# Kernel tuning notes

Measured on AMD Instinct MI355X. Metric: run time of the kernel, lower is better.

## Reference

```python
import jax, jax.numpy as jnp
import numpy as np

N = 50000
E = 800000
D = 16            # input_dim == hidden_dim == output_dim (required for consistency)
D2 = D * D
HEADS = 4
NEG_SLOPE = 0.2


def _gat_conv(x, src, dst, W, att_src, att_dst, bias):
    """PyG GATConv with concat=False (mean over heads), add_self_loops already applied.
    x: [N, Cin], W: [Cin, H*C], att_*: [H, C], bias: [C]."""
    H, C = att_src.shape
    xh = (x @ W).reshape(N, H, C)                     # [N, H, C]
    a_src = jnp.einsum('nhc,hc->nh', xh, att_src)      # [N, H]
    a_dst = jnp.einsum('nhc,hc->nh', xh, att_dst)
    alpha = jax.nn.leaky_relu(a_src[src] + a_dst[dst], NEG_SLOPE)   # [E, H]
    amax = jax.ops.segment_max(alpha, dst, num_segments=N)
    amax = jnp.where(jnp.isfinite(amax), amax, 0.0)
    ex = jnp.exp(alpha - jax.lax.stop_gradient(amax)[dst])
    denom = jax.ops.segment_sum(ex, dst, num_segments=N)
    coef = ex / (denom[dst] + 1e-16)                  # per-dst softmax over incoming edges
    acc = jnp.zeros((N, C), x.dtype)
    for h in range(H):  # loop over heads to avoid [E, H, C] intermediate
        acc = acc + jax.ops.segment_sum(coef[:, h:h + 1] * xh[src, h], dst, num_segments=N)
    return acc / H + bias


def setup_inputs() -> dict:
    key = jax.random.key(0)
    ks = jax.random.split(key, 20)
    s = lambda k, shape, fan: jax.random.normal(k, shape, jnp.float32) * (1.0 / np.sqrt(fan))
    inp = {
        'mean': jax.random.normal(ks[0], (N, D), jnp.float32),
        'cov': jax.random.normal(ks[1], (N, D, D), jnp.float32),
        'edge_index': jax.random.randint(ks[2], (2, E), 0, N, jnp.int32),
        # gat_mean params
        'W_mean': s(ks[3], (D, HEADS * D), D),
        'att_src_mean': s(ks[4], (HEADS, D), D),
        'att_dst_mean': s(ks[5], (HEADS, D), D),
        'bias_mean': jnp.zeros((D,), jnp.float32),
        # gat_cov params
        'W_cov': s(ks[6], (D2, HEADS * D2), D2),
        'att_src_cov': s(ks[7], (HEADS, D2), D2),
        'att_dst_cov': s(ks[8], (HEADS, D2), D2),
        'bias_cov': jnp.zeros((D2,), jnp.float32),
        # fc_mean: Linear(D,D) -> Linear(D,D)
        'fm_W1': s(ks[9], (D, D), D), 'fm_b1': jnp.zeros((D,), jnp.float32),
        'fm_W2': s(ks[10], (D, D), D), 'fm_b2': jnp.zeros((D,), jnp.float32),
        # fc_cov: Linear(D2,D2) -> Linear(D2,D2)
        'fcv_W1': s(ks[11], (D2, D2), D2), 'fcv_b1': jnp.zeros((D2,), jnp.float32),
        'fcv_W2': s(ks[12], (D2, D2), D2), 'fcv_b2': jnp.zeros((D2,), jnp.float32),
    }
    return inp


def reference(mean, cov, edge_index, W_mean, att_src_mean, att_dst_mean, bias_mean,
              W_cov, att_src_cov, att_dst_cov, bias_cov,
              fm_W1, fm_b1, fm_W2, fm_b2, fcv_W1, fcv_b1, fcv_W2, fcv_b2):
    loops = jnp.arange(N, dtype=edge_index.dtype)
    src = jnp.concatenate([edge_index[0], loops])
    dst = jnp.concatenate([edge_index[1], loops])

    cov_flat = cov.reshape(N, D2)
    mean_agg = _gat_conv(mean, src, dst, W_mean, att_src_mean, att_dst_mean, bias_mean)
    cov_agg = _gat_conv(cov_flat, src, dst, W_cov, att_src_cov, att_dst_cov, bias_cov)

    mean_out = (mean_agg @ fm_W1 + fm_b1) @ fm_W2 + fm_b2
    cov_out = (cov_agg @ fcv_W1 + fcv_b1) @ fcv_W2 + fcv_b2
    return mean_out, cov_out.reshape(N, D, D)
```

## Files before the change

### kernel.cpp

```cpp
#include <hip/hip_runtime.h>

#define NN 50000
#define EE 800000
#define DD 16
#define DD2 256
#define ETOT (EE + NN)
#define NB 196

typedef __bf16 bf16x8 __attribute__((ext_vector_type(8)));
typedef float f32x4 __attribute__((ext_vector_type(4)));
typedef float f32x2 __attribute__((ext_vector_type(2)));

__device__ inline unsigned short f2bf(float f) {
    unsigned int u = __float_as_uint(f);
    return (unsigned short)((u + 0x7FFFu + ((u >> 16) & 1u)) >> 16);
}

__device__ inline void gl2lds16(const void* g, void* l) {
    __builtin_amdgcn_global_load_lds((const __attribute__((address_space(1))) unsigned int*)g,
                                     (__attribute__((address_space(3))) unsigned int*)l, 16, 0, 0);
}

__global__ void k_count(const int* ei, int* counts) {
    int e = blockIdx.x * 256 + threadIdx.x;
    if (e < EE) atomicAdd(&counts[ei[EE + e]], 1);
}

__global__ void k_scan1(const int* counts, int* partial, int* bsum) {
    __shared__ int sh[256];
    int t = threadIdx.x;
    int n = blockIdx.x * 256 + t;
    int v = (n < NN) ? counts[n] + 1 : 0;
    sh[t] = v;
    __syncthreads();
    for (int d = 1; d < 256; d <<= 1) {
        int x = (t >= d) ? sh[t - d] : 0;
        __syncthreads();
        sh[t] += x;
        __syncthreads();
    }
    if (n < NN) partial[n] = sh[t];
    if (t == 255) bsum[blockIdx.x] = sh[255];
}

__global__ void k_scan3(const int* counts, const int* partial, const int* bsum,
                        int* row_start, int* cursor) {
    __shared__ int sh[256];
    int t = threadIdx.x;
    int v = (t < NB) ? bsum[t] : 0;
    sh[t] = v;
    __syncthreads();
    for (int d = 1; d < 256; d <<= 1) {
        int x = (t >= d) ? sh[t - d] : 0;
        __syncthreads();
        sh[t] += x;
        __syncthreads();
    }
    int boff = (blockIdx.x == 0) ? 0 : sh[blockIdx.x - 1];
    int n = blockIdx.x * 256 + t;
    if (n < NN) {
        int rs = partial[n] - (counts[n] + 1) + boff;
        row_start[n] = rs;
        cursor[n] = rs;
        if (n == NN - 1) row_start[NN] = partial[n] + boff;
    }
}

__global__ void k_scatter(const int* ei, int* cursor, int* srt) {
    int i = blockIdx.x * 256 + threadIdx.x;
    if (i >= ETOT) return;
    int s, d;
    if (i < EE) { s = ei[i]; d = ei[EE + i]; }
    else { s = d = i - EE; }
    int pos = atomicAdd(&cursor[d], 1);
    srt[pos] = s;
}

__global__ void k_pre(const float* fcv_W1, const float* fcv_W2, const float* fcv_b1, const float* fcv_b2,
                      const float* fm_W1, const float* fm_W2, const float* fm_b1, const float* fm_b2,
                      const float* W_cov, const float* as_cov, const float* ad_cov,
                      const float* W_mean, const float* as_mean, const float* ad_mean,
                      const float* bias_cov, const float* bias_mean,
                      unsigned short* WpT, float* bpc, float* vcov, float* vmean,
                      float* Wpm, float* bpm) {
    __shared__ float sh[256];
    int b = blockIdx.x, t = threadIdx.x;
    if (b < 1024) {
        int q = b >> 8, i = b & 255;
        const float* wrow = W_cov + (size_t)i * 1024 + q * 256;
        float t1 = 0.f;
        for (int j = 0; j < 256; ++j) t1 += wrow[j] * fcv_W1[j * 256 + t];
        sh[t] = t1;
        __syncthreads();
        float s = 0.f;
        for (int k = 0; k < 256; ++k) s += sh[k] * fcv_W2[k * 256 + t];
        int C = q * 32 + (i >> 3);
        int cs = C ^ (t & 7);
        WpT[(size_t)t * 1024 + cs * 8 + (i & 7)] = f2bf(0.25f * s);
    } else if (b == 1024) {
        float t1 = fcv_b1[t];
        for (int j = 0; j < 256; ++j) t1 += bias_cov[j] * fcv_W1[j * 256 + t];
        sh[t] = t1;
        __syncthreads();
        float s = fcv_b2[t];
        for (int k = 0; k < 256; ++k) s += sh[k] * fcv_W2[k * 256 + t];
        bpc[t] = s;
    } else if (b < 1033) {
        int ch = b - 1025, h = ch & 3;
        const float* att = (ch < 4) ? as_cov : ad_cov;
        int jl = t & 31, i8 = t >> 5;
        float av[8];
#pragma unroll
        for (int jj = 0; jj < 8; ++jj) av[jj] = att[h * 256 + jj * 32 + jl];
        for (int ii = 0; ii < 32; ++ii) {
            int i = ii * 8 + i8;
            const float* wr = W_cov + (size_t)i * 1024 + h * 256;
            float p = 0.f;
#pragma unroll
            for (int jj = 0; jj < 8; ++jj) p += wr[jj * 32 + jl] * av[jj];
#pragma unroll
            for (int off = 16; off; off >>= 1) p += __shfl_xor(p, off);
            if (jl == 0) vcov[ch * 256 + i] = p;
        }
    } else {
        {
            int j = t >> 4, c = t & 15;
            float s = 0.f;
            for (int k = 0; k < 16; ++k) s += fm_W1[j * 16 + k] * fm_W2[k * 16 + c];
            sh[j * 16 + c] = s;
        }
        if (t < 128) {
            int ch = t >> 4, i = t & 15, h = ch & 3;
            const float* att = (ch < 4) ? as_mean : ad_mean;
            float s = 0.f;
            for (int j = 0; j < 16; ++j) s += W_mean[i * 64 + h * 16 + j] * att[h * 16 + j];
            vmean[ch * 16 + i] = s;
        }
        __syncthreads();
#pragma unroll
        for (int r = 0; r < 4; ++r) {
            int idx = r * 256 + t;
            int k = idx >> 4, c = idx & 15, h = k >> 4, i = k & 15;
            float s = 0.f;
            for (int j = 0; j < 16; ++j) s += W_mean[i * 64 + h * 16 + j] * sh[j * 16 + c];
            Wpm[k * 16 + c] = 0.25f * s;
        }
        if (t < 16) {
            float b2 = fm_b2[t];
            for (int k = 0; k < 16; ++k) b2 += fm_b1[k] * fm_W2[k * 16 + t];
            float s = b2;
            for (int j = 0; j < 16; ++j) s += bias_mean[j] * sh[j * 16 + t];
            bpm[t] = s;
        }
    }
}

__global__ void __launch_bounds__(256) k_dots(const float* cov, const float* mean,
                                              const float* vcov, const float* vmean,
                                              float* asrc, float* adst, unsigned short* covb) {
    __shared__ float vc[8 * 256];
    __shared__ float vm[8 * 16];
    int t = threadIdx.x;
    for (int i = t; i < 2048; i += 256) vc[i] = vcov[i];
    if (t < 128) vm[t] = vmean[t];
    __syncthreads();
    int w = t >> 6, lane = t & 63;
    int n = blockIdx.x * 4 + w;
    float4 x = *(const float4*)(cov + (size_t)n * 256 + lane * 4);
    unsigned int u0 = (unsigned int)f2bf(x.x) | ((unsigned int)f2bf(x.y) << 16);
    unsigned int u1 = (unsigned int)f2bf(x.z) | ((unsigned int)f2bf(x.w) << 16);
    *(uint2*)((char*)covb + (size_t)n * 512 + lane * 8) = make_uint2(u0, u1);
    float p[8];
#pragma unroll
    for (int c = 0; c < 8; ++c) {
        float4 v = *(const float4*)&vc[c * 256 + lane * 4];
        p[c] = x.x * v.x + x.y * v.y + x.z * v.z + x.w * v.w;
    }
#pragma unroll
    for (int c = 0; c < 8; ++c)
        for (int off = 32; off; off >>= 1) p[c] += __shfl_xor(p[c], off);
    float xm = (lane < 16) ? mean[(size_t)n * 16 + lane] : 0.f;
    float q[8];
#pragma unroll
    for (int c = 0; c < 8; ++c) {
        q[c] = (lane < 16) ? xm * vm[c * 16 + lane] : 0.f;
        for (int off = 8; off; off >>= 1) q[c] += __shfl_xor(q[c], off);
    }
    if (lane == 0) {
        float4* ps = (float4*)(asrc + (size_t)n * 8);
        ps[0] = make_float4(p[0], p[1], p[2], p[3]);
        ps[1] = make_float4(q[0], q[1], q[2], q[3]);
        float4* pd = (float4*)(adst + (size_t)n * 8);
        pd[0] = make_float4(p[4], p[5], p[6], p[7]);
        pd[1] = make_float4(q[4], q[5], q[6], q[7]);
    }
}

__global__ void __launch_bounds__(256, 8) k_agg(const int* __restrict__ row_start, const int* __restrict__ srt,
                                                const float* __restrict__ asrc, const float* __restrict__ adst,
                                                const unsigned short* __restrict__ covb, const float* __restrict__ mean,
                                                unsigned short* __restrict__ Ycat, float* __restrict__ Ym) {
    __shared__ float exbuf[4][64][8];
    __shared__ float mrow[4][64][16];
    int t = threadIdx.x;
    int w = t >> 6, lane = t & 63;
    int ml = lane & 15;
    int hl4 = lane >> 4;
    const char* covbc = (const char*)covb;
    const char* meanc = (const char*)mean;
    const char* asrcc = (const char*)asrc;
    unsigned lodc = (unsigned)lane << 3;
    float* exw = &exbuf[w][0][0];
    float* mrw = &mrow[w][0][0];

    for (int n0 = blockIdx.x * 4; n0 < NN; n0 += gridDim.x * 4) {
        int nu = __builtin_amdgcn_readfirstlane(n0 + w);
        int beg = row_start[nu], deg = row_start[nu + 1] - beg;

        f32x2 acc[8];
#pragma unroll
        for (int k = 0; k < 8; ++k) acc[k] = (f32x2){0.f, 0.f};
        float accm = 0.f;
        float dsc[4] = {0, 0, 0, 0};
        float dsm = 0.f;

        auto loadg = [&](int jp, int s0v, uint2* cd) {
#pragma unroll
            for (int k2 = 0; k2 < 4; ++k2) {
                int se = __shfl(s0v, jp + k2);
                cd[k2] = *(const uint2*)(covbc + (((unsigned)se << 9) + lodc));
            }
        };
        auto compute4 = [&](int jp, const uint2* cd) {
#pragma unroll
            for (int k2 = 0; k2 < 4; ++k2) {
                int e = jp + k2;
                float4 e0 = *(const float4*)(exw + e * 8);
                float em = exw[e * 8 + 4 + hl4];
                float mv = mrw[e * 16 + (ml ^ ((e & 7) << 1))];
                f32x2 x0 = (f32x2){__uint_as_float(cd[k2].x << 16), __uint_as_float(cd[k2].x & 0xffff0000u)};
                f32x2 x1 = (f32x2){__uint_as_float(cd[k2].y << 16), __uint_as_float(cd[k2].y & 0xffff0000u)};
                float ev[4] = {e0.x, e0.y, e0.z, e0.w};
#pragma unroll
                for (int h = 0; h < 4; ++h) {
                    f32x2 e2 = (f32x2){ev[h], ev[h]};
                    acc[h * 2 + 0] = __builtin_elementwise_fma(e2, x0, acc[h * 2 + 0]);
                    acc[h * 2 + 1] = __builtin_elementwise_fma(e2, x1, acc[h * 2 + 1]);
                }
                dsc[0] += e0.x; dsc[1] += e0.y; dsc[2] += e0.z; dsc[3] += e0.w;
                accm += em * mv;
                dsm += em;
            }
        };

        for (int base = 0; base < deg; base += 64) {
            int i = base + lane;
            bool valid = i < deg;
            int s0 = srt[beg + (valid ? i : (deg - 1))];
            int cnt8 = (min(64, deg - base) + 7) & ~7;

            uint2 cdA[4], cdB[4];
            loadg(0, s0, cdA);
            loadg(4, s0, cdB);

            {
                const float4* pm = (const float4*)(meanc + ((size_t)((unsigned)s0 << 6)));
                bool oddE = lane & 1;
                int g0 = (lane >> 1) & 3;
                float* mb = mrw + lane * 16;
                float4 F0 = pm[0], F1 = pm[1];
                float4 V0 = oddE ? make_float4(F0.z, F0.w, F0.x, F0.y) : F0;
                float4 V1 = oddE ? make_float4(F1.z, F1.w, F1.x, F1.y) : F1;
                *(float4*)(mb + ((0 ^ g0) << 2)) = V0;
                *(float4*)(mb + ((1 ^ g0) << 2)) = V1;
                float4 F2 = pm[2], F3 = pm[3];
                float4 V2 = oddE ? make_float4(F2.z, F2.w, F2.x, F2.y) : F2;
                float4 V3 = oddE ? make_float4(F3.z, F3.w, F3.x, F3.y) : F3;
                *(float4*)(mb + ((2 ^ g0) << 2)) = V2;
                *(float4*)(mb + ((3 ^ g0) << 2)) = V3;
            }

            {
                const float4* pa = (const float4*)(asrcc + ((size_t)((unsigned)s0 << 5)));
                float4 a0 = pa[0], a1 = pa[1];
                const float4* pd = (const float4*)(adst + (size_t)nu * 8);
                float4 d0 = pd[0], d1 = pd[1];
                float av[8] = {a0.x, a0.y, a0.z, a0.w, a1.x, a1.y, a1.z, a1.w};
                float ad[8] = {d0.x, d0.y, d0.z, d0.w, d1.x, d1.y, d1.z, d1.w};
                float ex8[8];
#pragma unroll
                for (int c = 0; c < 8; ++c) {
                    float al = av[c] + ad[c];
                    al = (al >= 0.f) ? al : 0.2f * al;
                    float e = __expf(al);
                    ex8[c] = valid ? e : 0.f;
                }
                *(float4*)(exw + lane * 8) = make_float4(ex8[0], ex8[1], ex8[2], ex8[3]);
                *(float4*)(exw + lane * 8 + 4) = make_float4(ex8[4], ex8[5], ex8[6], ex8[7]);
            }

            for (int jp = 0; jp < cnt8; jp += 8) {
                compute4(jp, cdA);
                if (jp + 8 < cnt8) loadg(jp + 8, s0, cdA);
                compute4(jp + 4, cdB);
                if (jp + 12 < cnt8) loadg(jp + 12, s0, cdB);
            }
        }

        float invc[4] = {1.f / (dsc[0] + 1e-16f), 1.f / (dsc[1] + 1e-16f),
                         1.f / (dsc[2] + 1e-16f), 1.f / (dsc[3] + 1e-16f)};
        float invm = 1.f / (dsm + 1e-16f);
        char* yrow = (char*)Ycat + (size_t)nu * 2048;
        int cbase = lane >> 1, hl = lane & 1, sw = nu & 7;
#pragma unroll
        for (int h = 0; h < 4; ++h) {
            float iv = invc[h];
            uint2 pk;
            pk.x = (unsigned int)f2bf(acc[h * 2 + 0].x * iv) | ((unsigned int)f2bf(acc[h * 2 + 0].y * iv) << 16);
            pk.y = (unsigned int)f2bf(acc[h * 2 + 1].x * iv) | ((unsigned int)f2bf(acc[h * 2 + 1].y * iv) << 16);
            int cs = (h * 32 + cbase) ^ sw;
            *(uint2*)(yrow + cs * 16 + hl * 8) = pk;
        }
        Ym[(size_t)nu * 64 + lane] = accm * invm;
    }
}

__global__ void __launch_bounds__(256) k_gemm(const unsigned short* Ycat, const unsigned short* WpT,
                                              const float* bpc, float* out_cov,
                                              const float* Ym, const float* Wpm, const float* bpm,
                                              float* out_mean) {
    __shared__ __align__(16) unsigned short As[128 * 64];
    __shared__ __align__(16) unsigned short Bs[128 * 64];
    int t = threadIdx.x;
    if (blockIdx.x >= 782) {
        float* wm = (float*)As;
        float* bmv = (float*)Bs;
        for (int i = t; i < 1024; i += 256) wm[i] = Wpm[i];
        if (t < 16) bmv[t] = bpm[t];
        __syncthreads();
        int base = (blockIdx.x - 782) * 256;
        int c = t & 15;
#pragma unroll
        for (int p = 0; p < 16; ++p) {
            int node = base + p * 16 + (t >> 4);
            if (node < NN) {
                const float* yr = Ym + (size_t)node * 64;
                float s = bmv[c];
#pragma unroll
                for (int k = 0; k < 64; ++k) s += yr[k] * wm[k * 16 + c];
                out_mean[(size_t)node * 16 + c] = s;
            }
        }
        return;
    }
    int m0 = (blockIdx.x >> 1) * 128, c0 = (blockIdx.x & 1) * 128;
    int w = t >> 6, lane = t & 63;
    int mg = w >> 1, ng = w & 1;
    int q = lane >> 4, lm = lane & 15;
    f32x4 acc[4][4];
#pragma unroll
    for (int mt = 0; mt < 4; ++mt)
#pragma unroll
        for (int nt = 0; nt < 4; ++nt) acc[mt][nt] = (f32x4){0.f, 0.f, 0.f, 0.f};

    for (int kc = 0; kc < 16; ++kc) {
        int k0 = kc * 64;
#pragma unroll
        for (int i2 = 0; i2 < 4; ++i2) {
            int idx = t + i2 * 256;
            int row = idx >> 3, seg = idx & 7;
            int gm = m0 + row;
            if (gm < NN)
                gl2lds16(Ycat + (size_t)gm * 1024 + k0 + seg * 8, As + idx * 8);
        }
#pragma unroll
        for (int i2 = 0; i2 < 4; ++i2) {
            int idx = t + i2 * 256;
            int col = idx >> 3, seg = idx & 7;
            gl2lds16(WpT + (size_t)(c0 + col) * 1024 + k0 + seg * 8, Bs + idx * 8);
        }
        __syncthreads();
#pragma unroll
        for (int ks = 0; ks < 2; ++ks) {
            bf16x8 af[4], bfr[4];
#pragma unroll
            for (int mt = 0; mt < 4; ++mt) {
                int row = mg * 64 + mt * 16 + lm;
                int ch = (ks * 4 + q) ^ (row & 7);
                af[mt] = *(const bf16x8*)(As + row * 64 + ch * 8);
            }
#pragma unroll
            for (int nt = 0; nt < 4; ++nt) {
                int col = ng * 64 + nt * 16 + lm;
                int ch = (ks * 4 + q) ^ (col & 7);
                bfr[nt] = *(const bf16x8*)(Bs + col * 64 + ch * 8);
            }
#pragma unroll
            for (int mt = 0; mt < 4; ++mt)
#pragma unroll
                for (int nt = 0; nt < 4; ++nt)
                    acc[mt][nt] = __builtin_amdgcn_mfma_f32_16x16x32_bf16(af[mt], bfr[nt], acc[mt][nt], 0, 0, 0);
        }
        __syncthreads();
    }
#pragma unroll
    for (int nt = 0; nt < 4; ++nt) {
        int col = c0 + ng * 64 + nt * 16 + lm;
        float bias = bpc[col];
#pragma unroll
        for (int mt = 0; mt < 4; ++mt) {
#pragma unroll
            for (int e = 0; e < 4; ++e) {
                int r = m0 + mg * 64 + mt * 16 + q * 4 + e;
                if (r < NN)
                    __builtin_nontemporal_store(acc[mt][nt][e] + bias, &out_cov[(size_t)r * 256 + col]);
            }
        }
    }
}

extern "C" void kernel_launch(void* const* d_in, const int* in_sizes, int n_in,
                              void* d_out, int out_size, void* d_ws, size_t ws_size,
                              hipStream_t stream) {
    const float* mean = (const float*)d_in[0];
    const float* cov = (const float*)d_in[1];
    const int* ei = (const int*)d_in[2];
    const float* W_mean = (const float*)d_in[3];
    const float* as_mean = (const float*)d_in[4];
    const float* ad_mean = (const float*)d_in[5];
    const float* bias_mean = (const float*)d_in[6];
    const float* W_cov = (const float*)d_in[7];
    const float* as_cov = (const float*)d_in[8];
    const float* ad_cov = (const float*)d_in[9];
    const float* bias_cov = (const float*)d_in[10];
    const float* fm_W1 = (const float*)d_in[11];
    const float* fm_b1 = (const float*)d_in[12];
    const float* fm_W2 = (const float*)d_in[13];
    const float* fm_b2 = (const float*)d_in[14];
    const float* fcv_W1 = (const float*)d_in[15];
    const float* fcv_b1 = (const float*)d_in[16];
    const float* fcv_W2 = (const float*)d_in[17];
    const float* fcv_b2 = (const float*)d_in[18];

    float* out_mean = (float*)d_out;
    float* out_cov = (float*)d_out + (size_t)NN * DD;

    char* w = (char*)d_ws;
    auto alloc = [&](size_t bytes) -> void* {
        void* p = (void*)w;
        w += (bytes + 255) & ~(size_t)255;
        return p;
    };
    unsigned short* Ycat = (unsigned short*)alloc((size_t)NN * 1024 * 2);
    unsigned short* covb = (unsigned short*)alloc((size_t)NN * 256 * 2);
    float* Ym = (float*)alloc((size_t)NN * 64 * 4);
    int* counts = (int*)alloc(NN * 4);
    int* partial = (int*)alloc(NN * 4);
    int* bsum = (int*)alloc(256 * 4);
    int* row_start = (int*)alloc((NN + 1) * 4);
    int* cursor = (int*)alloc(NN * 4);
    int* srt = (int*)alloc((size_t)ETOT * 4);
    float* asrc = (float*)alloc((size_t)NN * 8 * 4);
    float* adst = (float*)alloc((size_t)NN * 8 * 4);
    float* vcov = (float*)alloc(8 * 256 * 4);
    float* vmean = (float*)alloc(8 * 16 * 4);
    unsigned short* WpT = (unsigned short*)alloc(256 * 1024 * 2);
    float* bpc = (float*)alloc(256 * 4);
    float* Wpm = (float*)alloc(64 * 16 * 4);
    float* bpm = (float*)alloc(16 * 4);

    hipMemsetAsync(counts, 0, NN * 4, stream);
    k_count<<<(EE + 255) / 256, 256, 0, stream>>>(ei, counts);
    k_scan1<<<NB, 256, 0, stream>>>(counts, partial, bsum);
    k_scan3<<<NB, 256, 0, stream>>>(counts, partial, bsum, row_start, cursor);
    k_scatter<<<(ETOT + 255) / 256, 256, 0, stream>>>(ei, cursor, srt);
    k_pre<<<1034, 256, 0, stream>>>(fcv_W1, fcv_W2, fcv_b1, fcv_b2, fm_W1, fm_W2, fm_b1, fm_b2,
                                    W_cov, as_cov, ad_cov, W_mean, as_mean, ad_mean,
                                    bias_cov, bias_mean, WpT, bpc, vcov, vmean, Wpm, bpm);
    k_dots<<<NN / 4, 256, 0, stream>>>(cov, mean, vcov, vmean, asrc, adst, covb);
    k_agg<<<1536, 256, 0, stream>>>(row_start, srt, asrc, adst, covb, mean, Ycat, Ym);
    k_gemm<<<782 + 196, 256, 0, stream>>>(Ycat, WpT, bpc, out_cov, Ym, Wpm, bpm, out_mean);
}
```

Before: 453.3 us.

## Merge count/scatter into pre/dots launches and widen GEMM tile to full N

The edge-count atomics are folded into the weight-precompute kernel as extra blocks, and the CSR scatter is folded into the dots kernel as extra blocks, cutting two kernel launches and letting independent work overlap. The cov GEMM now computes all 256 output columns per block (8 N-tiles per wave, 32 accumulators), so each Ycat A-tile is loaded once instead of twice. The cost is more register pressure and double the B LDS footprint in the GEMM, which may lower occupancy. The blocks that run the merged count and scatter work have no dependence on the rest of their kernel.

```diff
diff --git a/kernel.cpp b/kernel.cpp
--- a/kernel.cpp
+++ b/kernel.cpp
@@ -19,11 +19,6 @@
 __device__ inline void gl2lds16(const void* g, void* l) {
     __builtin_amdgcn_global_load_lds((const __attribute__((address_space(1))) unsigned int*)g,
                                      (__attribute__((address_space(3))) unsigned int*)l, 16, 0, 0);
-}
-
-__global__ void k_count(const int* ei, int* counts) {
-    int e = blockIdx.x * 256 + threadIdx.x;
-    if (e < EE) atomicAdd(&counts[ei[EE + e]], 1);
 }
 
 __global__ void k_scan1(const int* counts, int* partial, int* bsum) {
@@ -66,25 +61,20 @@
     }
 }
 
-__global__ void k_scatter(const int* ei, int* cursor, int* srt) {
-    int i = blockIdx.x * 256 + threadIdx.x;
-    if (i >= ETOT) return;
-    int s, d;
-    if (i < EE) { s = ei[i]; d = ei[EE + i]; }
-    else { s = d = i - EE; }
-    int pos = atomicAdd(&cursor[d], 1);
-    srt[pos] = s;
-}
-
-__global__ void k_pre(const float* fcv_W1, const float* fcv_W2, const float* fcv_b1, const float* fcv_b2,
-                      const float* fm_W1, const float* fm_W2, const float* fm_b1, const float* fm_b2,
-                      const float* W_cov, const float* as_cov, const float* ad_cov,
-                      const float* W_mean, const float* as_mean, const float* ad_mean,
-                      const float* bias_cov, const float* bias_mean,
-                      unsigned short* WpT, float* bpc, float* vcov, float* vmean,
-                      float* Wpm, float* bpm) {
+__global__ void k_cnt_pre(const float* fcv_W1, const float* fcv_W2, const float* fcv_b1, const float* fcv_b2,
+                          const float* fm_W1, const float* fm_W2, const float* fm_b1, const float* fm_b2,
+                          const float* W_cov, const float* as_cov, const float* ad_cov,
+                          const float* W_mean, const float* as_mean, const float* ad_mean,
+                          const float* bias_cov, const float* bias_mean,
+                          unsigned short* WpT, float* bpc, float* vcov, float* vmean,
+                          float* Wpm, float* bpm, const int* ei, int* counts) {
     __shared__ float sh[256];
     int b = blockIdx.x, t = threadIdx.x;
+    if (b >= 1034) {
+        int e = (b - 1034) * 256 + t;
+        if (e < EE) atomicAdd(&counts[ei[EE + e]], 1);
+        return;
+    }
     if (b < 1024) {
         int q = b >> 8, i = b & 255;
         const float* wrow = W_cov + (size_t)i * 1024 + q * 256;
@@ -155,12 +145,24 @@
     }
 }
 
-__global__ void __launch_bounds__(256) k_dots(const float* cov, const float* mean,
-                                              const float* vcov, const float* vmean,
-                                              float* asrc, float* adst, unsigned short* covb) {
+__global__ void __launch_bounds__(256) k_scat_dots(const float* cov, const float* mean,
+                                                   const float* vcov, const float* vmean,
+                                                   float* asrc, float* adst, unsigned short* covb,
+                                                   const int* ei, int* cursor, int* srt) {
     __shared__ float vc[8 * 256];
     __shared__ float vm[8 * 16];
     int t = threadIdx.x;
+    if (blockIdx.x >= 12500) {
+        int i = (blockIdx.x - 12500) * 256 + t;
+        if (i < ETOT) {
+            int s, d;
+            if (i < EE) { s = ei[i]; d = ei[EE + i]; }
+            else { s = d = i - EE; }
+            int pos = atomicAdd(&cursor[d], 1);
+            srt[pos] = s;
+        }
+        return;
+    }
     for (int i = t; i < 2048; i += 256) vc[i] = vcov[i];
     if (t < 128) vm[t] = vmean[t];
     __syncthreads();
@@ -330,15 +332,15 @@
                                               const float* Ym, const float* Wpm, const float* bpm,
                                               float* out_mean) {
     __shared__ __align__(16) unsigned short As[128 * 64];
-    __shared__ __align__(16) unsigned short Bs[128 * 64];
+    __shared__ __align__(16) unsigned short Bs[256 * 64];
     int t = threadIdx.x;
-    if (blockIdx.x >= 782) {
+    if (blockIdx.x >= 391) {
         float* wm = (float*)As;
         float* bmv = (float*)Bs;
         for (int i = t; i < 1024; i += 256) wm[i] = Wpm[i];
         if (t < 16) bmv[t] = bpm[t];
         __syncthreads();
-        int base = (blockIdx.x - 782) * 256;
+        int base = (blockIdx.x - 391) * 256;
         int c = t & 15;
 #pragma unroll
         for (int p = 0; p < 16; ++p) {
@@ -353,15 +355,15 @@
         }
         return;
     }
-    int m0 = (blockIdx.x >> 1) * 128, c0 = (blockIdx.x & 1) * 128;
+    int m0 = blockIdx.x * 128;
     int w = t >> 6, lane = t & 63;
     int mg = w >> 1, ng = w & 1;
     int q = lane >> 4, lm = lane & 15;
-    f32x4 acc[4][4];
+    f32x4 acc[4][8];
 #pragma unroll
     for (int mt = 0; mt < 4; ++mt)
 #pragma unroll
-        for (int nt = 0; nt < 4; ++nt) acc[mt][nt] = (f32x4){0.f, 0.f, 0.f, 0.f};
+        for (int nt = 0; nt < 8; ++nt) acc[mt][nt] = (f32x4){0.f, 0.f, 0.f, 0.f};
 
     for (int kc = 0; kc < 16; ++kc) {
         int k0 = kc * 64;
@@ -374,15 +376,15 @@
                 gl2lds16(Ycat + (size_t)gm * 1024 + k0 + seg * 8, As + idx * 8);
         }
 #pragma unroll
-        for (int i2 = 0; i2 < 4; ++i2) {
+        for (int i2 = 0; i2 < 8; ++i2) {
             int idx = t + i2 * 256;
             int col = idx >> 3, seg = idx & 7;
-            gl2lds16(WpT + (size_t)(c0 + col) * 1024 + k0 + seg * 8, Bs + idx * 8);
+            gl2lds16(WpT + (size_t)col * 1024 + k0 + seg * 8, Bs + idx * 8);
         }
         __syncthreads();
 #pragma unroll
         for (int ks = 0; ks < 2; ++ks) {
-            bf16x8 af[4], bfr[4];
+            bf16x8 af[4], bfr[8];
 #pragma unroll
             for (int mt = 0; mt < 4; ++mt) {
                 int row = mg * 64 + mt * 16 + lm;
@@ -390,22 +392,22 @@
                 af[mt] = *(const bf16x8*)(As + row * 64 + ch * 8);
             }
 #pragma unroll
-            for (int nt = 0; nt < 4; ++nt) {
-                int col = ng * 64 + nt * 16 + lm;
+            for (int nt = 0; nt < 8; ++nt) {
+                int col = ng * 128 + nt * 16 + lm;
                 int ch = (ks * 4 + q) ^ (col & 7);
                 bfr[nt] = *(const bf16x8*)(Bs + col * 64 + ch * 8);
             }
 #pragma unroll
             for (int mt = 0; mt < 4; ++mt)
 #pragma unroll
-                for (int nt = 0; nt < 4; ++nt)
+                for (int nt = 0; nt < 8; ++nt)
                     acc[mt][nt] = __builtin_amdgcn_mfma_f32_16x16x32_bf16(af[mt], bfr[nt], acc[mt][nt], 0, 0, 0);
         }
         __syncthreads();
     }
 #pragma unroll
-    for (int nt = 0; nt < 4; ++nt) {
-        int col = c0 + ng * 64 + nt * 16 + lm;
+    for (int nt = 0; nt < 8; ++nt) {
+        int col = ng * 128 + nt * 16 + lm;
         float bias = bpc[col];
 #pragma unroll
         for (int mt = 0; mt < 4; ++mt) {
@@ -470,14 +472,14 @@
     float* bpm = (float*)alloc(16 * 4);
 
     hipMemsetAsync(counts, 0, NN * 4, stream);
-    k_count<<<(EE + 255) / 256, 256, 0, stream>>>(ei, counts);
+    k_cnt_pre<<<1034 + 3125, 256, 0, stream>>>(fcv_W1, fcv_W2, fcv_b1, fcv_b2, fm_W1, fm_W2, fm_b1, fm_b2,
+                                               W_cov, as_cov, ad_cov, W_mean, as_mean, ad_mean,
+                                               bias_cov, bias_mean, WpT, bpc, vcov, vmean, Wpm, bpm,
+                                               ei, counts);
     k_scan1<<<NB, 256, 0, stream>>>(counts, partial, bsum);
     k_scan3<<<NB, 256, 0, stream>>>(counts, partial, bsum, row_start, cursor);
-    k_scatter<<<(ETOT + 255) / 256, 256, 0, stream>>>(ei, cursor, srt);
-    k_pre<<<1034, 256, 0, stream>>>(fcv_W1, fcv_W2, fcv_b1, fcv_b2, fm_W1, fm_W2, fm_b1, fm_b2,
-                                    W_cov, as_cov, ad_cov, W_mean, as_mean, ad_mean,
-                                    bias_cov, bias_mean, WpT, bpc, vcov, vmean, Wpm, bpm);
-    k_dots<<<NN / 4, 256, 0, stream>>>(cov, mean, vcov, vmean, asrc, adst, covb);
+    k_scat_dots<<<12500 + 3321, 256, 0, stream>>>(cov, mean, vcov, vmean, asrc, adst, covb,
+                                                  ei, cursor, srt);
     k_agg<<<1536, 256, 0, stream>>>(row_start, srt, asrc, adst, covb, mean, Ycat, Ym);
-    k_gemm<<<782 + 196, 256, 0, stream>>>(Ycat, WpT, bpc, out_cov, Ym, Wpm, bpm, out_mean);
-}
+    k_gemm<<<391 + 196, 256, 0, stream>>>(Ycat, WpT, bpc, out_cov, Ym, Wpm, bpm, out_mean);
+}
```

Result: slower. 469.6 us (+3.6%).
